# Performance work log

Hardware: AMD Instinct MI355X
Metric: run time of the kernel (lower is better)

Reference implementation:

```python
import jax, jax.numpy as jnp
import numpy as np

N = 100_000      # nodes
E = 1_600_000    # edges
B = 256          # graphs
DIM = 64
EPS = 1e-5


def _batchnorm(h, gamma, beta):
    # BatchNorm1d in training mode: batch mean, biased variance
    mu = jnp.mean(h, axis=0)
    var = jnp.mean((h - mu) ** 2, axis=0)
    return (h - mu) * jax.lax.rsqrt(var + EPS) * gamma + beta


def setup_inputs() -> dict:
    key = jax.random.key(0)
    ks = jax.random.split(key, 12)
    x = jax.random.normal(ks[0], (N, DIM), dtype=jnp.float32)
    edge_index = jax.random.randint(ks[1], (2, E), 0, N, dtype=jnp.int64)
    edge_attr = jax.random.normal(ks[2], (E, DIM), dtype=jnp.float32)
    state = jax.random.normal(ks[3], (B, DIM), dtype=jnp.float32)
    batch = jnp.sort(jax.random.randint(ks[4], (N,), 0, B, dtype=jnp.int64))
    s = 0.05
    params = {
        "W1": jax.random.normal(ks[5], (DIM, 3 * DIM), dtype=jnp.float32) * s,
        "b1": jnp.zeros((DIM,), jnp.float32),
        "g1": jnp.ones((DIM,), jnp.float32),
        "be1": jnp.zeros((DIM,), jnp.float32),
        "W2": jax.random.normal(ks[6], (DIM, DIM), dtype=jnp.float32) * s,
        "b2": jnp.zeros((DIM,), jnp.float32),
        "g2": jnp.ones((DIM,), jnp.float32),
        "be2": jnp.zeros((DIM,), jnp.float32),
        "W3": jax.random.normal(ks[7], (DIM, DIM), dtype=jnp.float32) * s,
        "b3": jnp.zeros((DIM,), jnp.float32),
        "g3": jnp.ones((DIM,), jnp.float32),
        "be3": jnp.zeros((DIM,), jnp.float32),
    }
    return {"x": x, "edge_index": edge_index, "edge_attr": edge_attr,
            "state": state, "batch": batch, **params}


def reference(x, edge_index, edge_attr, state, batch,
              W1, b1, g1, be1, W2, b2, g2, be2, W3, b3, g3, be3):
    n = x.shape[0]
    src = edge_index[0]
    # scatter-mean of edge_attr onto destination-of-src nodes
    sums = jax.ops.segment_sum(edge_attr, src, num_segments=n)
    cnt = jax.ops.segment_sum(jnp.ones((edge_attr.shape[0],), edge_attr.dtype),
                              src, num_segments=n)
    v_mean = sums / jnp.maximum(cnt, 1.0)[:, None]
    comb = jnp.concatenate([x, v_mean, state[batch]], axis=1)  # [N, 3*DIM]
    h = jax.nn.relu(comb @ W1.T + b1)
    h = _batchnorm(h, g1, be1)
    h = jax.nn.relu(h @ W2.T + b2)
    h = _batchnorm(h, g2, be2)
    h = h @ W3.T + b3
    return _batchnorm(h, g3, be3)
```

## Files before the change

### kernel.cpp

```cpp
#include <hip/hip_runtime.h>

#define NN 100000
#define NE 1600000
#define EPSV 1e-5f

typedef float f32x4 __attribute__((ext_vector_type(4)));
typedef short s16x8 __attribute__((ext_vector_type(8)));

__device__ __forceinline__ unsigned short f2bf(float f) {
  unsigned int u = __float_as_uint(f);
  u += 0x7fffu + ((u >> 16) & 1u);
  return (unsigned short)(u >> 16);
}

__device__ __forceinline__ float bf2f(unsigned short s) {
  return __uint_as_float(((unsigned int)s) << 16);
}

__device__ __forceinline__ ushort4 pack4(float4 v) {
  ushort4 s;
  s.x = f2bf(v.x); s.y = f2bf(v.y); s.z = f2bf(v.z); s.w = f2bf(v.w);
  return s;
}

__global__ __launch_bounds__(256) void k_bucket(
    const int* __restrict__ ei, int* __restrict__ cnt, int* __restrict__ eids) {
  int e = blockIdx.x * 256 + threadIdx.x;
  int src = ei[e];
  int pos = atomicAdd(&cnt[src], 1);
  if (pos < 64) eids[(size_t)src * 64 + pos] = e;
}

__global__ __launch_bounds__(256) void k_gather(
    const int* __restrict__ cnt, const int* __restrict__ eids,
    const float4* __restrict__ ea4, ushort4* __restrict__ vmb4) {
  int wid = (blockIdx.x * 256 + threadIdx.x) >> 6;
  int lane = threadIdx.x & 63;
  int grp = lane >> 4, q = lane & 15;
  int n0 = wid * 13;
  int nend = n0 + 13 < NN ? n0 + 13 : NN;
  for (int n = n0; n < nend; ++n) {
    const int* elist = eids + (size_t)n * 64;
    int c = cnt[n];
    int m = c < 64 ? c : 64;
    int rm = m - 1;
    float ax = 0.f, ay = 0.f, az = 0.f, aw = 0.f;
    {
      int r0 = grp,      r1 = 4 + grp,  r2 = 8 + grp,  r3 = 12 + grp;
      int r4 = 16 + grp, r5 = 20 + grp, r6 = 24 + grp, r7 = 28 + grp;
      int i0 = elist[r0 < m ? r0 : rm];
      int i1 = elist[r1 < m ? r1 : rm];
      int i2 = elist[r2 < m ? r2 : rm];
      int i3 = elist[r3 < m ? r3 : rm];
      int i4 = elist[r4 < m ? r4 : rm];
      int i5 = elist[r5 < m ? r5 : rm];
      int i6 = elist[r6 < m ? r6 : rm];
      int i7 = elist[r7 < m ? r7 : rm];
      float4 v0 = ea4[(size_t)i0 * 16 + q];
      float4 v1 = ea4[(size_t)i1 * 16 + q];
      float4 v2 = ea4[(size_t)i2 * 16 + q];
      float4 v3 = ea4[(size_t)i3 * 16 + q];
      float4 v4 = ea4[(size_t)i4 * 16 + q];
      float4 v5 = ea4[(size_t)i5 * 16 + q];
      float4 v6 = ea4[(size_t)i6 * 16 + q];
      float4 v7 = ea4[(size_t)i7 * 16 + q];
      float m0 = r0 < m ? 1.f : 0.f, m1 = r1 < m ? 1.f : 0.f;
      float m2 = r2 < m ? 1.f : 0.f, m3 = r3 < m ? 1.f : 0.f;
      ax += m0 * v0.x + m1 * v1.x + m2 * v2.x + m3 * v3.x;
      ay += m0 * v0.y + m1 * v1.y + m2 * v2.y + m3 * v3.y;
      az += m0 * v0.z + m1 * v1.z + m2 * v2.z + m3 * v3.z;
      aw += m0 * v0.w + m1 * v1.w + m2 * v2.w + m3 * v3.w;
      float m4 = r4 < m ? 1.f : 0.f, m5 = r5 < m ? 1.f : 0.f;
      float m6 = r6 < m ? 1.f : 0.f, m7 = r7 < m ? 1.f : 0.f;
      ax += m4 * v4.x + m5 * v5.x + m6 * v6.x + m7 * v7.x;
      ay += m4 * v4.y + m5 * v5.y + m6 * v6.y + m7 * v7.y;
      az += m4 * v4.z + m5 * v5.z + m6 * v6.z + m7 * v7.z;
      aw += m4 * v4.w + m5 * v5.w + m6 * v6.w + m7 * v7.w;
    }
    if (m > 32) {
      for (int e = 32; e < m; e += 16) {
        int r0 = e + grp, r1 = e + 4 + grp, r2 = e + 8 + grp, r3 = e + 12 + grp;
        int i0 = elist[r0 < m ? r0 : rm];
        int i1 = elist[r1 < m ? r1 : rm];
        int i2 = elist[r2 < m ? r2 : rm];
        int i3 = elist[r3 < m ? r3 : rm];
        float4 v0 = ea4[(size_t)i0 * 16 + q];
        float4 v1 = ea4[(size_t)i1 * 16 + q];
        float4 v2 = ea4[(size_t)i2 * 16 + q];
        float4 v3 = ea4[(size_t)i3 * 16 + q];
        float m0 = r0 < m ? 1.f : 0.f, m1 = r1 < m ? 1.f : 0.f;
        float m2 = r2 < m ? 1.f : 0.f, m3 = r3 < m ? 1.f : 0.f;
        ax += m0 * v0.x + m1 * v1.x + m2 * v2.x + m3 * v3.x;
        ay += m0 * v0.y + m1 * v1.y + m2 * v2.y + m3 * v3.y;
        az += m0 * v0.z + m1 * v1.z + m2 * v2.z + m3 * v3.z;
        aw += m0 * v0.w + m1 * v1.w + m2 * v2.w + m3 * v3.w;
      }
    }
    ax += __shfl_xor(ax, 16); ay += __shfl_xor(ay, 16);
    az += __shfl_xor(az, 16); aw += __shfl_xor(aw, 16);
    ax += __shfl_xor(ax, 32); ay += __shfl_xor(ay, 32);
    az += __shfl_xor(az, 32); aw += __shfl_xor(aw, 32);
    if (lane < 16) {
      float inv = 1.0f / fmaxf((float)c, 1.0f);
      float4 r; r.x = ax * inv; r.y = ay * inv; r.z = az * inv; r.w = aw * inv;
      vmb4[(size_t)n * 16 + lane] = pack4(r);
    }
  }
}

__global__ __launch_bounds__(256) void k_g1(
    const float4* __restrict__ x4, const ushort4* __restrict__ vmb4,
    const float4* __restrict__ state4,
    const int* __restrict__ batch, const float4* __restrict__ w14,
    const float* __restrict__ b1, unsigned short* __restrict__ h1,
    float* __restrict__ Sout, float* __restrict__ Qout) {
  __shared__ unsigned short lc[64][200];
  __shared__ unsigned short lw[64][200];
  __shared__ float ssum[64], ssq[64];
  const int tid = threadIdx.x;
  const int nodeBase = blockIdx.x * 64;
  if (tid < 64) { ssum[tid] = 0.f; ssq[tid] = 0.f; }
#pragma unroll
  for (int i = 0; i < 12; ++i) {
    int idx = tid + i * 256;
    int row = idx / 48, q = idx % 48;
    *(ushort4*)&lw[row][q * 4] = pack4(w14[idx]);
  }
#pragma unroll
  for (int i = 0; i < 4; ++i) {
    int idx = tid + i * 256;
    int node = idx >> 4, q = idx & 15;
    int g = nodeBase + node;
    float4 vx = {0,0,0,0}, vs = {0,0,0,0};
    ushort4 vm = {0,0,0,0};
    if (g < NN) {
      vx = x4[(size_t)g * 16 + q];
      vm = vmb4[(size_t)g * 16 + q];
      int b = batch[g];
      vs = state4[b * 16 + q];
    }
    *(ushort4*)&lc[node][q * 4]       = pack4(vx);
    *(ushort4*)&lc[node][64 + q * 4]  = vm;
    *(ushort4*)&lc[node][128 + q * 4] = pack4(vs);
  }
  __syncthreads();
  const int lane = tid & 63, w = tid >> 6;
  const int rg = lane >> 4, ci = lane & 15;
  f32x4 acc[4] = {{0,0,0,0},{0,0,0,0},{0,0,0,0},{0,0,0,0}};
#pragma unroll
  for (int s = 0; s < 6; ++s) {
    int k0 = 32 * s + rg * 8;
    s16x8 a = *(const s16x8*)&lc[w * 16 + ci][k0];
#pragma unroll
    for (int c = 0; c < 4; ++c) {
      s16x8 b = *(const s16x8*)&lw[c * 16 + ci][k0];
      acc[c] = __builtin_amdgcn_mfma_f32_16x16x32_bf16(a, b, acc[c], 0, 0, 0);
    }
  }
  __syncthreads();
  unsigned short (*lo)[72] = (unsigned short(*)[72])lw;
#pragma unroll
  for (int c = 0; c < 4; ++c) {
    int col = c * 16 + ci;
    float bb = b1[col];
    float ls = 0.f, lq = 0.f;
#pragma unroll
    for (int r = 0; r < 4; ++r) {
      int row = w * 16 + rg * 4 + r;
      float v = fmaxf(acc[c][r] + bb, 0.f);
      lo[row][col] = f2bf(v);
      if (nodeBase + row < NN) { ls += v; lq += v * v; }
    }
    atomicAdd(&ssum[col], ls);
    atomicAdd(&ssq[col], lq);
  }
  __syncthreads();
#pragma unroll
  for (int i = 0; i < 2; ++i) {
    int idx = tid + i * 256;
    int row = idx >> 3, q = idx & 7;
    int g = nodeBase + row;
    if (g < NN) *(s16x8*)&h1[(size_t)g * 64 + q * 8] = *(const s16x8*)&lo[row][q * 8];
  }
  if (tid < 64) {
    unsafeAtomicAdd(&Sout[tid], ssum[tid]);
    unsafeAtomicAdd(&Qout[tid], ssq[tid]);
  }
}

__global__ __launch_bounds__(256) void k_prep(
    const float* __restrict__ Sin, const float* __restrict__ Qin,
    const float* __restrict__ gm, const float* __restrict__ bt,
    const float* __restrict__ W, const float* __restrict__ bias,
    unsigned short* __restrict__ wf, float* __restrict__ dout) {
  __shared__ float lA[64], lC[64], red[256];
  int t = threadIdx.x;
  if (t < 64) {
    float mu = Sin[t] * (1.0f / NN);
    float var = Qin[t] * (1.0f / NN) - mu * mu;
    float a = gm[t] * rsqrtf(var + EPSV);
    lA[t] = a;
    lC[t] = bt[t] - mu * a;
  }
  __syncthreads();
#pragma unroll
  for (int i = 0; i < 16; ++i) {
    int idx = t + i * 256;
    wf[idx] = f2bf(W[idx] * lA[idx & 63]);
  }
  int j = t >> 2, p = t & 3;
  const float* Wr = W + j * 64 + p * 16;
  float s = 0.f;
#pragma unroll
  for (int k = 0; k < 16; ++k) s += lC[p * 16 + k] * Wr[k];
  red[t] = s;
  __syncthreads();
  if (t < 64) dout[t] = bias[t] + red[t * 4] + red[t * 4 + 1] + red[t * 4 + 2] + red[t * 4 + 3];
}

template <bool RELU>
__global__ __launch_bounds__(256) void k_gemm64(
    const s16x8* __restrict__ A8,
    const s16x8* __restrict__ w8,
    const float* __restrict__ d,
    unsigned short* __restrict__ Obf,
    float* __restrict__ Sout, float* __restrict__ Qout) {
  __shared__ unsigned short la[64][72];
  __shared__ unsigned short lwf[64][72];
  __shared__ float ssum[64], ssq[64];
  const int tid = threadIdx.x;
  const int nodeBase = blockIdx.x * 64;
  if (tid < 64) { ssum[tid] = 0.f; ssq[tid] = 0.f; }
#pragma unroll
  for (int i = 0; i < 2; ++i) {
    int idx = tid + i * 256;
    int row = idx >> 3, q = idx & 7;
    int g = nodeBase + row;
    s16x8 v = {};
    if (g < NN) v = A8[(size_t)g * 8 + q];
    *(s16x8*)&la[row][q * 8] = v;
  }
#pragma unroll
  for (int i = 0; i < 2; ++i) {
    int idx = tid + i * 256;
    int j = idx >> 3, q = idx & 7;
    *(s16x8*)&lwf[j][q * 8] = w8[idx];
  }
  __syncthreads();
  const int lane = tid & 63, w = tid >> 6;
  const int rg = lane >> 4, ci = lane & 15;
  f32x4 acc[4] = {{0,0,0,0},{0,0,0,0},{0,0,0,0},{0,0,0,0}};
#pragma unroll
  for (int s = 0; s < 2; ++s) {
    int k0 = 32 * s + rg * 8;
    s16x8 a = *(const s16x8*)&la[w * 16 + ci][k0];
#pragma unroll
    for (int c = 0; c < 4; ++c) {
      s16x8 b = *(const s16x8*)&lwf[c * 16 + ci][k0];
      acc[c] = __builtin_amdgcn_mfma_f32_16x16x32_bf16(a, b, acc[c], 0, 0, 0);
    }
  }
  __syncthreads();
  unsigned short (*lo)[72] = (unsigned short(*)[72])la;
#pragma unroll
  for (int c = 0; c < 4; ++c) {
    int col = c * 16 + ci;
    float dd = d[col];
    float ls = 0.f, lq = 0.f;
#pragma unroll
    for (int r = 0; r < 4; ++r) {
      int row = w * 16 + rg * 4 + r;
      float v = acc[c][r] + dd;
      if (RELU) v = fmaxf(v, 0.f);
      lo[row][col] = f2bf(v);
      if (nodeBase + row < NN) { ls += v; lq += v * v; }
    }
    atomicAdd(&ssum[col], ls);
    atomicAdd(&ssq[col], lq);
  }
  __syncthreads();
#pragma unroll
  for (int i = 0; i < 2; ++i) {
    int idx = tid + i * 256;
    int row = idx >> 3, q = idx & 7;
    int g = nodeBase + row;
    if (g < NN) *(s16x8*)&Obf[(size_t)g * 64 + q * 8] = *(const s16x8*)&lo[row][q * 8];
  }
  if (tid < 64) {
    unsafeAtomicAdd(&Sout[tid], ssum[tid]);
    unsafeAtomicAdd(&Qout[tid], ssq[tid]);
  }
}

__global__ __launch_bounds__(256) void k_bn3(
    const s16x8* __restrict__ h3b, const float* __restrict__ gm,
    const float* __restrict__ bt, const float* __restrict__ S,
    const float* __restrict__ Q, float4* __restrict__ out) {
  __shared__ float lA[64], lC[64];
  const int tid = threadIdx.x;
  if (tid < 64) {
    float mu = S[tid] * (1.0f / NN);
    float var = Q[tid] * (1.0f / NN) - mu * mu;
    float a = gm[tid] * rsqrtf(var + EPSV);
    lA[tid] = a;
    lC[tid] = bt[tid] - mu * a;
  }
  __syncthreads();
  const int total = NN * 8;
  for (int idx = blockIdx.x * 256 + tid; idx < total; idx += gridDim.x * 256) {
    s16x8 v = h3b[idx];
    int k = (idx & 7) * 8;
    float4 o0, o1;
    o0.x = bf2f((unsigned short)v[0]) * lA[k]     + lC[k];
    o0.y = bf2f((unsigned short)v[1]) * lA[k + 1] + lC[k + 1];
    o0.z = bf2f((unsigned short)v[2]) * lA[k + 2] + lC[k + 2];
    o0.w = bf2f((unsigned short)v[3]) * lA[k + 3] + lC[k + 3];
    o1.x = bf2f((unsigned short)v[4]) * lA[k + 4] + lC[k + 4];
    o1.y = bf2f((unsigned short)v[5]) * lA[k + 5] + lC[k + 5];
    o1.z = bf2f((unsigned short)v[6]) * lA[k + 6] + lC[k + 6];
    o1.w = bf2f((unsigned short)v[7]) * lA[k + 7] + lC[k + 7];
    out[idx * 2]     = o0;
    out[idx * 2 + 1] = o1;
  }
}

extern "C" void kernel_launch(void* const* d_in, const int* in_sizes, int n_in,
                              void* d_out, int out_size, void* d_ws, size_t ws_size,
                              hipStream_t stream) {
  const float* x     = (const float*)d_in[0];
  const int*   ei    = (const int*)d_in[1];
  const float* ea    = (const float*)d_in[2];
  const float* state = (const float*)d_in[3];
  const int*   batch = (const int*)d_in[4];
  const float* W1  = (const float*)d_in[5];
  const float* b1  = (const float*)d_in[6];
  const float* g1  = (const float*)d_in[7];
  const float* be1 = (const float*)d_in[8];
  const float* W2  = (const float*)d_in[9];
  const float* b2  = (const float*)d_in[10];
  const float* g2  = (const float*)d_in[11];
  const float* be2 = (const float*)d_in[12];
  const float* W3  = (const float*)d_in[13];
  const float* b3  = (const float*)d_in[14];
  const float* g3  = (const float*)d_in[15];
  const float* be3 = (const float*)d_in[16];

  char* ws = (char*)d_ws;
  int*   cnt  = (int*)ws;
  float* S1   = (float*)(ws + 400000);
  float* Q1 = S1 + 64;
  float* S2 = S1 + 128;
  float* Q2 = S1 + 192;
  float* S3 = S1 + 256;
  float* Q3 = S1 + 320;
  unsigned short* w2f = (unsigned short*)(ws + 401536);
  float*          d2  = (float*)(ws + 409728);
  unsigned short* w3f = (unsigned short*)(ws + 409984);
  float*          d3  = (float*)(ws + 418176);
  int*            eids = (int*)(ws + 418432);
  unsigned short* h3b  = (unsigned short*)(ws + 418432);
  unsigned short* vmb  = (unsigned short*)(ws + 26018432);
  unsigned short* h2   = (unsigned short*)(ws + 26018432);
  unsigned short* h1   = (unsigned short*)(ws + 38818432);

  hipMemsetAsync(ws, 0, 401536, stream);

  k_bucket<<<NE / 256, 256, 0, stream>>>(ei, cnt, eids);
  k_gather<<<2048, 256, 0, stream>>>(cnt, eids, (const float4*)ea, (ushort4*)vmb);

  const int nblk = (NN + 63) / 64;
  k_g1<<<nblk, 256, 0, stream>>>((const float4*)x, (const ushort4*)vmb,
                                 (const float4*)state, batch, (const float4*)W1,
                                 b1, h1, S1, Q1);
  k_prep<<<1, 256, 0, stream>>>(S1, Q1, g1, be1, W2, b2, w2f, d2);
  k_gemm64<true><<<nblk, 256, 0, stream>>>(
      (const s16x8*)h1, (const s16x8*)w2f, d2, h2, S2, Q2);
  k_prep<<<1, 256, 0, stream>>>(S2, Q2, g2, be2, W3, b3, w3f, d3);
  k_gemm64<false><<<nblk, 256, 0, stream>>>(
      (const s16x8*)h2, (const s16x8*)w3f, d3, h3b, S3, Q3);
  k_bn3<<<2048, 256, 0, stream>>>((const s16x8*)h3b, g3, be3, S3, Q3, (float4*)d_out);
}
```

Baseline: 387.8 us.

## Overlap x/state GEMM with edge bucketing and fold BN prep into GEMMs

Splits the first GEMM so the x and state parts are computed by extra blocks interleaved into the edge-bucketing launch, storing fp32 partial accumulators, while a second kernel adds only the v_mean contribution after the gather. It also removes the single-block k_prep launches by having every GEMM block recompute the BN scale/shift, the scaled bf16 weights and the folded bias itself. This cuts two serial launches and overlaps compute with the atomic-bound bucketing. In exchange it writes and rereads a 25MB fp32 partial buffer and repeats the weight folding in every block.

Result: faster. 363.8 us (-6.2%).

```diff
diff --git a/kernel.cpp b/kernel.cpp
--- a/kernel.cpp
+++ b/kernel.cpp
@@ -3,6 +3,7 @@
 #define NN 100000
 #define NE 1600000
 #define EPSV 1e-5f
+#define NTILE 1563
 
 typedef float f32x4 __attribute__((ext_vector_type(4)));
 typedef short s16x8 __attribute__((ext_vector_type(8)));
@@ -23,12 +24,64 @@
   return s;
 }
 
-__global__ __launch_bounds__(256) void k_bucket(
-    const int* __restrict__ ei, int* __restrict__ cnt, int* __restrict__ eids) {
-  int e = blockIdx.x * 256 + threadIdx.x;
-  int src = ei[e];
-  int pos = atomicAdd(&cnt[src], 1);
-  if (pos < 64) eids[(size_t)src * 64 + pos] = e;
+__global__ __launch_bounds__(256) void k_bucket_g1a(
+    const int* __restrict__ ei, int* __restrict__ cnt, int* __restrict__ eids,
+    const float4* __restrict__ x4, const float4* __restrict__ state4,
+    const int* __restrict__ batch, const float4* __restrict__ w14,
+    f32x4* __restrict__ ph) {
+  __shared__ unsigned short lx[64][136];
+  __shared__ unsigned short lw[64][136];
+  const int idx = blockIdx.x;
+  const int tid = threadIdx.x;
+  const bool is_g1a = ((idx % 5) == 2) && (idx / 5 < NTILE);
+  if (!is_g1a) {
+    int nga = idx / 5 + (((idx % 5) > 2) ? 1 : 0);
+    if (nga > NTILE) nga = NTILE;
+    int e = (idx - nga) * 256 + tid;
+    int src = ei[e];
+    int pos = atomicAdd(&cnt[src], 1);
+    if (pos < 64) eids[(size_t)src * 64 + pos] = e;
+    return;
+  }
+  const int tile = idx / 5;
+  const int nodeBase = tile * 64;
+#pragma unroll
+  for (int i = 0; i < 4; ++i) {
+    int t = tid + i * 256;
+    int j = t >> 4, q = t & 15;
+    *(ushort4*)&lw[j][q * 4]      = pack4(w14[j * 48 + q]);
+    *(ushort4*)&lw[j][64 + q * 4] = pack4(w14[j * 48 + 32 + q]);
+  }
+#pragma unroll
+  for (int i = 0; i < 4; ++i) {
+    int t = tid + i * 256;
+    int node = t >> 4, q = t & 15;
+    int g = nodeBase + node;
+    float4 vx = {0,0,0,0}, vs = {0,0,0,0};
+    if (g < NN) {
+      vx = x4[(size_t)g * 16 + q];
+      vs = state4[batch[g] * 16 + q];
+    }
+    *(ushort4*)&lx[node][q * 4]      = pack4(vx);
+    *(ushort4*)&lx[node][64 + q * 4] = pack4(vs);
+  }
+  __syncthreads();
+  const int lane = tid & 63, w = tid >> 6;
+  const int rg = lane >> 4, ci = lane & 15;
+  f32x4 acc[4] = {{0,0,0,0},{0,0,0,0},{0,0,0,0},{0,0,0,0}};
+#pragma unroll
+  for (int s = 0; s < 4; ++s) {
+    int k0 = 32 * s + rg * 8;
+    s16x8 a = *(const s16x8*)&lx[w * 16 + ci][k0];
+#pragma unroll
+    for (int c = 0; c < 4; ++c) {
+      s16x8 b = *(const s16x8*)&lw[c * 16 + ci][k0];
+      acc[c] = __builtin_amdgcn_mfma_f32_16x16x32_bf16(a, b, acc[c], 0, 0, 0);
+    }
+  }
+#pragma unroll
+  for (int c = 0; c < 4; ++c)
+    ph[(size_t)tile * 1024 + tid * 4 + c] = acc[c];
 }
 
 __global__ __launch_bounds__(256) void k_gather(
@@ -108,57 +161,46 @@
   }
 }
 
-__global__ __launch_bounds__(256) void k_g1(
-    const float4* __restrict__ x4, const ushort4* __restrict__ vmb4,
-    const float4* __restrict__ state4,
-    const int* __restrict__ batch, const float4* __restrict__ w14,
-    const float* __restrict__ b1, unsigned short* __restrict__ h1,
+__global__ __launch_bounds__(256) void k_g1b(
+    const ushort4* __restrict__ vmb4, const float4* __restrict__ w14,
+    const float* __restrict__ b1, const f32x4* __restrict__ ph,
+    unsigned short* __restrict__ h1,
     float* __restrict__ Sout, float* __restrict__ Qout) {
-  __shared__ unsigned short lc[64][200];
-  __shared__ unsigned short lw[64][200];
+  __shared__ unsigned short lv[64][72];
+  __shared__ unsigned short lwv[64][72];
   __shared__ float ssum[64], ssq[64];
   const int tid = threadIdx.x;
-  const int nodeBase = blockIdx.x * 64;
+  const int tile = blockIdx.x;
+  const int nodeBase = tile * 64;
   if (tid < 64) { ssum[tid] = 0.f; ssq[tid] = 0.f; }
 #pragma unroll
-  for (int i = 0; i < 12; ++i) {
-    int idx = tid + i * 256;
-    int row = idx / 48, q = idx % 48;
-    *(ushort4*)&lw[row][q * 4] = pack4(w14[idx]);
-  }
-#pragma unroll
   for (int i = 0; i < 4; ++i) {
-    int idx = tid + i * 256;
-    int node = idx >> 4, q = idx & 15;
-    int g = nodeBase + node;
-    float4 vx = {0,0,0,0}, vs = {0,0,0,0};
+    int t = tid + i * 256;
+    int j = t >> 4, q = t & 15;
+    *(ushort4*)&lwv[j][q * 4] = pack4(w14[j * 48 + 16 + q]);
+    int g = nodeBase + j;
     ushort4 vm = {0,0,0,0};
-    if (g < NN) {
-      vx = x4[(size_t)g * 16 + q];
-      vm = vmb4[(size_t)g * 16 + q];
-      int b = batch[g];
-      vs = state4[b * 16 + q];
-    }
-    *(ushort4*)&lc[node][q * 4]       = pack4(vx);
-    *(ushort4*)&lc[node][64 + q * 4]  = vm;
-    *(ushort4*)&lc[node][128 + q * 4] = pack4(vs);
+    if (g < NN) vm = vmb4[(size_t)g * 16 + q];
+    *(ushort4*)&lv[j][q * 4] = vm;
   }
   __syncthreads();
   const int lane = tid & 63, w = tid >> 6;
   const int rg = lane >> 4, ci = lane & 15;
-  f32x4 acc[4] = {{0,0,0,0},{0,0,0,0},{0,0,0,0},{0,0,0,0}};
-#pragma unroll
-  for (int s = 0; s < 6; ++s) {
+  f32x4 acc[4];
+#pragma unroll
+  for (int c = 0; c < 4; ++c) acc[c] = ph[(size_t)tile * 1024 + tid * 4 + c];
+#pragma unroll
+  for (int s = 0; s < 2; ++s) {
     int k0 = 32 * s + rg * 8;
-    s16x8 a = *(const s16x8*)&lc[w * 16 + ci][k0];
+    s16x8 a = *(const s16x8*)&lv[w * 16 + ci][k0];
 #pragma unroll
     for (int c = 0; c < 4; ++c) {
-      s16x8 b = *(const s16x8*)&lw[c * 16 + ci][k0];
+      s16x8 b = *(const s16x8*)&lwv[c * 16 + ci][k0];
       acc[c] = __builtin_amdgcn_mfma_f32_16x16x32_bf16(a, b, acc[c], 0, 0, 0);
     }
   }
   __syncthreads();
-  unsigned short (*lo)[72] = (unsigned short(*)[72])lw;
+  unsigned short (*lo)[72] = (unsigned short(*)[72])lwv;
 #pragma unroll
   for (int c = 0; c < 4; ++c) {
     int col = c * 16 + ci;
@@ -177,8 +219,8 @@
   __syncthreads();
 #pragma unroll
   for (int i = 0; i < 2; ++i) {
-    int idx = tid + i * 256;
-    int row = idx >> 3, q = idx & 7;
+    int t = tid + i * 256;
+    int row = t >> 3, q = t & 7;
     int g = nodeBase + row;
     if (g < NN) *(s16x8*)&h1[(size_t)g * 64 + q * 8] = *(const s16x8*)&lo[row][q * 8];
   }
@@ -188,64 +230,52 @@
   }
 }
 
-__global__ __launch_bounds__(256) void k_prep(
+template <bool RELU>
+__global__ __launch_bounds__(256) void k_gemm64f(
+    const s16x8* __restrict__ A8,
+    const float* __restrict__ Wf,
+    const float* __restrict__ bias,
+    const float* __restrict__ gm, const float* __restrict__ bt,
     const float* __restrict__ Sin, const float* __restrict__ Qin,
-    const float* __restrict__ gm, const float* __restrict__ bt,
-    const float* __restrict__ W, const float* __restrict__ bias,
-    unsigned short* __restrict__ wf, float* __restrict__ dout) {
-  __shared__ float lA[64], lC[64], red[256];
-  int t = threadIdx.x;
-  if (t < 64) {
-    float mu = Sin[t] * (1.0f / NN);
-    float var = Qin[t] * (1.0f / NN) - mu * mu;
-    float a = gm[t] * rsqrtf(var + EPSV);
-    lA[t] = a;
-    lC[t] = bt[t] - mu * a;
-  }
-  __syncthreads();
-#pragma unroll
-  for (int i = 0; i < 16; ++i) {
-    int idx = t + i * 256;
-    wf[idx] = f2bf(W[idx] * lA[idx & 63]);
-  }
-  int j = t >> 2, p = t & 3;
-  const float* Wr = W + j * 64 + p * 16;
-  float s = 0.f;
-#pragma unroll
-  for (int k = 0; k < 16; ++k) s += lC[p * 16 + k] * Wr[k];
-  red[t] = s;
-  __syncthreads();
-  if (t < 64) dout[t] = bias[t] + red[t * 4] + red[t * 4 + 1] + red[t * 4 + 2] + red[t * 4 + 3];
-}
-
-template <bool RELU>
-__global__ __launch_bounds__(256) void k_gemm64(
-    const s16x8* __restrict__ A8,
-    const s16x8* __restrict__ w8,
-    const float* __restrict__ d,
     unsigned short* __restrict__ Obf,
     float* __restrict__ Sout, float* __restrict__ Qout) {
   __shared__ unsigned short la[64][72];
   __shared__ unsigned short lwf[64][72];
-  __shared__ float ssum[64], ssq[64];
+  __shared__ float lA[64], lC[64], ld[64], red[256], ssum[64], ssq[64];
   const int tid = threadIdx.x;
   const int nodeBase = blockIdx.x * 64;
-  if (tid < 64) { ssum[tid] = 0.f; ssq[tid] = 0.f; }
+  if (tid < 64) {
+    float mu = Sin[tid] * (1.0f / NN);
+    float var = Qin[tid] * (1.0f / NN) - mu * mu;
+    float a = gm[tid] * rsqrtf(var + EPSV);
+    lA[tid] = a; lC[tid] = bt[tid] - mu * a;
+    ssum[tid] = 0.f; ssq[tid] = 0.f;
+  }
+  __syncthreads();
 #pragma unroll
   for (int i = 0; i < 2; ++i) {
-    int idx = tid + i * 256;
-    int row = idx >> 3, q = idx & 7;
+    int t = tid + i * 256;
+    int row = t >> 3, q = t & 7;
     int g = nodeBase + row;
     s16x8 v = {};
     if (g < NN) v = A8[(size_t)g * 8 + q];
     *(s16x8*)&la[row][q * 8] = v;
   }
 #pragma unroll
-  for (int i = 0; i < 2; ++i) {
-    int idx = tid + i * 256;
-    int j = idx >> 3, q = idx & 7;
-    *(s16x8*)&lwf[j][q * 8] = w8[idx];
-  }
+  for (int i = 0; i < 16; ++i) {
+    int t = tid + i * 256;
+    lwf[t >> 6][t & 63] = f2bf(Wf[t] * lA[t & 63]);
+  }
+  {
+    int j = tid >> 2, p = tid & 3;
+    const float* Wr = Wf + j * 64 + p * 16;
+    float s = 0.f;
+#pragma unroll
+    for (int k = 0; k < 16; ++k) s += lC[p * 16 + k] * Wr[k];
+    red[tid] = s;
+  }
+  __syncthreads();
+  if (tid < 64) ld[tid] = bias[tid] + red[tid*4] + red[tid*4+1] + red[tid*4+2] + red[tid*4+3];
   __syncthreads();
   const int lane = tid & 63, w = tid >> 6;
   const int rg = lane >> 4, ci = lane & 15;
@@ -265,7 +295,7 @@
 #pragma unroll
   for (int c = 0; c < 4; ++c) {
     int col = c * 16 + ci;
-    float dd = d[col];
+    float dd = ld[col];
     float ls = 0.f, lq = 0.f;
 #pragma unroll
     for (int r = 0; r < 4; ++r) {
@@ -281,8 +311,8 @@
   __syncthreads();
 #pragma unroll
   for (int i = 0; i < 2; ++i) {
-    int idx = tid + i * 256;
-    int row = idx >> 3, q = idx & 7;
+    int t = tid + i * 256;
+    int row = t >> 3, q = t & 7;
     int g = nodeBase + row;
     if (g < NN) *(s16x8*)&Obf[(size_t)g * 64 + q * 8] = *(const s16x8*)&lo[row][q * 8];
   }
@@ -353,30 +383,24 @@
   float* Q2 = S1 + 192;
   float* S3 = S1 + 256;
   float* Q3 = S1 + 320;
-  unsigned short* w2f = (unsigned short*)(ws + 401536);
-  float*          d2  = (float*)(ws + 409728);
-  unsigned short* w3f = (unsigned short*)(ws + 409984);
-  float*          d3  = (float*)(ws + 418176);
-  int*            eids = (int*)(ws + 418432);
-  unsigned short* h3b  = (unsigned short*)(ws + 418432);
+  int*            eids = (int*)(ws + 401536);
+  unsigned short* h3b  = (unsigned short*)(ws + 401536);
   unsigned short* vmb  = (unsigned short*)(ws + 26018432);
   unsigned short* h2   = (unsigned short*)(ws + 26018432);
   unsigned short* h1   = (unsigned short*)(ws + 38818432);
+  f32x4*          ph   = (f32x4*)(ws + 51618432);
 
   hipMemsetAsync(ws, 0, 401536, stream);
 
-  k_bucket<<<NE / 256, 256, 0, stream>>>(ei, cnt, eids);
+  k_bucket_g1a<<<6250 + NTILE, 256, 0, stream>>>(
+      ei, cnt, eids, (const float4*)x, (const float4*)state, batch,
+      (const float4*)W1, ph);
   k_gather<<<2048, 256, 0, stream>>>(cnt, eids, (const float4*)ea, (ushort4*)vmb);
-
-  const int nblk = (NN + 63) / 64;
-  k_g1<<<nblk, 256, 0, stream>>>((const float4*)x, (const ushort4*)vmb,
-                                 (const float4*)state, batch, (const float4*)W1,
-                                 b1, h1, S1, Q1);
-  k_prep<<<1, 256, 0, stream>>>(S1, Q1, g1, be1, W2, b2, w2f, d2);
-  k_gemm64<true><<<nblk, 256, 0, stream>>>(
-      (const s16x8*)h1, (const s16x8*)w2f, d2, h2, S2, Q2);
-  k_prep<<<1, 256, 0, stream>>>(S2, Q2, g2, be2, W3, b3, w3f, d3);
-  k_gemm64<false><<<nblk, 256, 0, stream>>>(
-      (const s16x8*)h2, (const s16x8*)w3f, d3, h3b, S3, Q3);
+  k_g1b<<<NTILE, 256, 0, stream>>>((const ushort4*)vmb, (const float4*)W1,
+                                   b1, ph, h1, S1, Q1);
+  k_gemm64f<true><<<NTILE, 256, 0, stream>>>(
+      (const s16x8*)h1, W2, b2, g1, be1, S1, Q1, h2, S2, Q2);
+  k_gemm64f<false><<<NTILE, 256, 0, stream>>>(
+      (const s16x8*)h2, W3, b3, g2, be2, S2, Q2, h3b, S3, Q3);
   k_bn3<<<2048, 256, 0, stream>>>((const s16x8*)h3b, g3, be3, S3, Q3, (float4*)d_out);
 }
```
